# Performance work log

Measured on AMD Instinct MI355X. Metric: run time of the kernel, lower is better.

The kernel has to match this reference:

```python
import jax, jax.numpy as jnp
import numpy as np

N = 100000
E = 1600000
IN_C, HID_C, OUT_C = 512, 256, 64
K = 10
ALPHA = 0.1


def setup_inputs() -> dict:
    key = jax.random.key(0)
    k1, k2, k3, k4 = jax.random.split(key, 4)
    x = jax.random.normal(k1, (N, IN_C), dtype=jnp.float32)
    edge_index = jax.random.randint(k2, (2, E), 0, N, dtype=jnp.int64)
    # Glorot-ish scaled linear weights
    W1 = jax.random.normal(k3, (HID_C, IN_C), dtype=jnp.float32) / np.sqrt(IN_C)
    b1 = jnp.zeros((HID_C,), dtype=jnp.float32)
    W2 = jax.random.normal(k4, (OUT_C, HID_C), dtype=jnp.float32) / np.sqrt(HID_C)
    b2 = jnp.zeros((OUT_C,), dtype=jnp.float32)
    # PPR init: temp[k] = alpha*(1-alpha)^k, temp[K] = (1-alpha)^K
    temp = ALPHA * (1.0 - ALPHA) ** np.arange(K + 1)
    temp[-1] = (1.0 - ALPHA) ** K
    temp = jnp.asarray(temp, dtype=jnp.float32)
    return {"x": x, "edge_index": edge_index, "W1": W1, "b1": b1,
            "W2": W2, "b2": b2, "temp": temp}


def _gcn_norm(edge_index, num_nodes):
    # add self loops with weight 1, symmetric normalization D^-1/2 A D^-1/2
    loop = jnp.arange(num_nodes, dtype=edge_index.dtype)
    src = jnp.concatenate([edge_index[0], loop])
    dst = jnp.concatenate([edge_index[1], loop])
    w = jnp.ones(src.shape[0], dtype=jnp.float32)
    deg = jax.ops.segment_sum(w, dst, num_segments=num_nodes)
    dinv = jnp.where(deg > 0, jax.lax.rsqrt(deg), 0.0)
    norm = dinv[src] * w * dinv[dst]
    return src, dst, norm


def reference(x, edge_index, W1, b1, W2, b2, temp):
    # MLP (inference mode: dropout is identity)
    h = jax.nn.relu(x @ W1.T + b1)
    h = h @ W2.T + b2  # [N, OUT_C]

    src, dst, norm = _gcn_norm(edge_index, N)
    norm = norm[:, None]

    def step(carry, gamma):
        xk, hidden = carry
        xk = jax.ops.segment_sum(norm * xk[src], dst, num_segments=N)
        hidden = hidden + gamma * xk
        return (xk, hidden), None

    hidden0 = temp[0] * h
    (_, hidden), _ = jax.lax.scan(step, (h, hidden0), temp[1:])
    return hidden
```

## Files before the change

### kernel.cpp

```cpp
#include <hip/hip_runtime.h>

#define IN_C   512
#define HID_C  256
#define OUT_C  64
#define KSTEPS 10

typedef __attribute__((ext_vector_type(8))) short bf16x8;
typedef __attribute__((ext_vector_type(4))) float f32x4;

__device__ __forceinline__ uint f2bf(float f) {
    uint u = __float_as_uint(f);
    return (u + 0x7fffu + ((u >> 16) & 1u)) >> 16;
}
__device__ __forceinline__ float bfl(uint u) { return __uint_as_float(u << 16); }
__device__ __forceinline__ float bfh(uint u) { return __uint_as_float(u & 0xffff0000u); }

__global__ void k_init(int* __restrict__ cnt, int* __restrict__ fill, int n) {
    int i = blockIdx.x * blockDim.x + threadIdx.x;
    if (i < n) { cnt[i] = 0; fill[i] = 0; }
}

__global__ void k_hist(const int* __restrict__ ei, int* __restrict__ cnt, int E) {
    int e = blockIdx.x * blockDim.x + threadIdx.x;
    if (e < E) atomicAdd(&cnt[ei[E + e]], 1);
}

__global__ void k_dinv(const int* __restrict__ cnt, float* __restrict__ dinv, int n) {
    int i = blockIdx.x * blockDim.x + threadIdx.x;
    if (i < n) dinv[i] = rsqrtf((float)cnt[i] + 1.0f);
}

__global__ void k_scan1(const int* __restrict__ cnt, int* __restrict__ rowptr,
                        int* __restrict__ bsum, int n) {
    __shared__ int sh[256];
    int i = blockIdx.x * 256 + threadIdx.x;
    int v = (i < n) ? cnt[i] : 0;
    sh[threadIdx.x] = v;
    __syncthreads();
    for (int off = 1; off < 256; off <<= 1) {
        int t = (threadIdx.x >= off) ? sh[threadIdx.x - off] : 0;
        __syncthreads();
        sh[threadIdx.x] += t;
        __syncthreads();
    }
    if (i < n) rowptr[i + 1] = sh[threadIdx.x];
    if (threadIdx.x == 255) bsum[blockIdx.x] = sh[255];
}

__global__ void k_scan2(int* __restrict__ bsum, int nb) {
    __shared__ int sh[512];
    int t = threadIdx.x;
    int v = (t < nb) ? bsum[t] : 0;
    sh[t] = v;
    __syncthreads();
    for (int off = 1; off < 512; off <<= 1) {
        int u = (t >= off) ? sh[t - off] : 0;
        __syncthreads();
        sh[t] += u;
        __syncthreads();
    }
    int ex = (t == 0) ? 0 : sh[t - 1];
    if (t < nb) bsum[t] = ex;
}

__global__ void k_scan3(int* __restrict__ rowptr, const int* __restrict__ bsum, int n) {
    int i = blockIdx.x * blockDim.x + threadIdx.x;
    if (i < n) rowptr[i + 1] += bsum[i >> 8];
    if (i == 0) rowptr[0] = 0;
}

__global__ void k_scatter(const int* __restrict__ ei, const float* __restrict__ dinv,
                          const int* __restrict__ rowptr, int* __restrict__ fill,
                          int2* __restrict__ edges, int E) {
    int e = blockIdx.x * blockDim.x + threadIdx.x;
    if (e < E) {
        int s = ei[e], d = ei[E + e];
        float nv = dinv[s] * dinv[d];
        int pos = rowptr[d] + atomicAdd(&fill[d], 1);
        edges[pos] = make_int2(s, __float_as_int(nv));
    }
}

__global__ void k_cvt(const float* __restrict__ src, ushort* __restrict__ dst, int n) {
    int i = blockIdx.x * blockDim.x + threadIdx.x;
    if (i < n) dst[i] = (ushort)f2bf(src[i]);
}

__global__ __launch_bounds__(256, 4) void k_mlp(
    const float* __restrict__ x, const ushort* __restrict__ W1b,
    const float* __restrict__ b1, const ushort* __restrict__ W2b,
    const float* __restrict__ b2, const float* __restrict__ temp,
    ushort* __restrict__ h, float* __restrict__ out, int n)
{
    __shared__ uint4 smem4[2560];
    char* smem = (char*)smem4;

    const int tid = threadIdx.x;
    const int lane = tid & 63;
    const int w    = tid >> 6;
    const int l15  = lane & 15;
    const int l4   = lane >> 4;
    const int row0 = blockIdx.x * 64;

    f32x4 acc[4][4];
#pragma unroll
    for (int i = 0; i < 4; ++i)
#pragma unroll
        for (int j = 0; j < 4; ++j) acc[i][j] = (f32x4){0.f, 0.f, 0.f, 0.f};

    for (int k0 = 0; k0 < IN_C; k0 += 64) {
#pragma unroll
        for (int it = 0; it < 4; ++it) {
            int f  = tid + it * 256;
            int r  = f >> 4;
            int c4 = f & 15;
            int gr = row0 + r; if (gr >= n) gr = n - 1;
            float4 v = *(const float4*)(x + (size_t)gr * IN_C + k0 + c4 * 4);
            uint p0 = f2bf(v.x) | (f2bf(v.y) << 16);
            uint p1 = f2bf(v.z) | (f2bf(v.w) << 16);
            int boff = (c4 * 8) ^ ((r & 7) << 4);
            *(uint2*)(smem + 32768 + r * 128 + boff) = make_uint2(p0, p1);
        }
#pragma unroll
        for (int it = 0; it < 8; ++it) {
            int m  = tid + it * 256;
            int nn = m >> 3, b = m & 7;
            uint4 v = *(const uint4*)(W1b + (size_t)nn * IN_C + k0 + b * 8);
            int bd = b ^ (nn & 7);
            *(uint4*)(smem + nn * 128 + (bd << 4)) = v;
        }
        __syncthreads();
#pragma unroll
        for (int kk = 0; kk < 2; ++kk) {
            bf16x8 af[4], bfr[4];
            int kb = kk * 4 + l4;
#pragma unroll
            for (int rf = 0; rf < 4; ++rf) {
                int r = rf * 16 + l15;
                af[rf] = *(const bf16x8*)(smem + 32768 + r * 128 + ((kb ^ (r & 7)) << 4));
            }
#pragma unroll
            for (int nf = 0; nf < 4; ++nf) {
                int nn = w * 64 + nf * 16 + l15;
                bfr[nf] = *(const bf16x8*)(smem + nn * 128 + ((kb ^ (nn & 7)) << 4));
            }
#pragma unroll
            for (int rf = 0; rf < 4; ++rf)
#pragma unroll
                for (int nf = 0; nf < 4; ++nf)
                    acc[rf][nf] = __builtin_amdgcn_mfma_f32_16x16x32_bf16(
                        af[rf], bfr[nf], acc[rf][nf], 0, 0, 0);
        }
        __syncthreads();
    }

    float bias1[4];
#pragma unroll
    for (int nf = 0; nf < 4; ++nf) bias1[nf] = b1[w * 64 + nf * 16 + l15];
#pragma unroll
    for (int rf = 0; rf < 4; ++rf)
#pragma unroll
        for (int nf = 0; nf < 4; ++nf)
#pragma unroll
            for (int j = 0; j < 4; ++j) {
                int r = rf * 16 + l4 * 4 + j;
                int c = w * 64 + nf * 16 + l15;
                float v = fmaxf(acc[rf][nf][j] + bias1[nf], 0.f);
                int byte = r * 512 + ((((c >> 3) ^ (r & 7))) << 4) + (c & 7) * 2;
                *(ushort*)(smem + byte) = (ushort)f2bf(v);
            }
    __syncthreads();

    f32x4 acc2[4];
#pragma unroll
    for (int nf = 0; nf < 4; ++nf) acc2[nf] = (f32x4){0.f, 0.f, 0.f, 0.f};
#pragma unroll
    for (int kk = 0; kk < 8; ++kk) {
        int r = w * 16 + l15;
        int kb = kk * 4 + l4;
        bf16x8 a = *(const bf16x8*)(smem + r * 512 + ((kb ^ (r & 7)) << 4));
#pragma unroll
        for (int nf = 0; nf < 4; ++nf) {
            bf16x8 bb = *(const bf16x8*)(W2b + (size_t)(nf * 16 + l15) * HID_C + kb * 8);
            acc2[nf] = __builtin_amdgcn_mfma_f32_16x16x32_bf16(a, bb, acc2[nf], 0, 0, 0);
        }
    }

    float t0 = temp[0];
#pragma unroll
    for (int nf = 0; nf < 4; ++nf) {
        int c = nf * 16 + l15;
        float bias = b2[c];
#pragma unroll
        for (int j = 0; j < 4; ++j) {
            int gr = row0 + w * 16 + l4 * 4 + j;
            if (gr < n) {
                float v = acc2[nf][j] + bias;
                h[(size_t)gr * OUT_C + c]   = (ushort)f2bf(v);
                out[(size_t)gr * OUT_C + c] = t0 * v;
            }
        }
    }
}

__global__ __launch_bounds__(256) void k_prop(
    const int* __restrict__ rowptr, const int2* __restrict__ edges,
    const ushort* __restrict__ cur, ushort* __restrict__ nxt,
    float* __restrict__ out, const float* __restrict__ dinv,
    const float* __restrict__ temp, int k, int n)
{
    const int lane = threadIdx.x & 63;
    const int g    = lane >> 3;
    const int sl   = lane & 7;
    const int wid  = (blockIdx.x * blockDim.x + threadIdx.x) >> 6;
    const int nw   = (gridDim.x * blockDim.x) >> 6;
    const float gamma = temp[k];

    for (int d = wid; d < n; d += nw) {
        const int b = rowptr[d], en = rowptr[d + 1];
        const float di = dinv[d];
        float a[8] = {0.f, 0.f, 0.f, 0.f, 0.f, 0.f, 0.f, 0.f};

        if (g == 0) {
            uint4 raw = *(const uint4*)(cur + (size_t)d * OUT_C + sl * 8);
            float s = di * di;
            a[0] = s * bfl(raw.x); a[1] = s * bfh(raw.x);
            a[2] = s * bfl(raw.y); a[3] = s * bfh(raw.y);
            a[4] = s * bfl(raw.z); a[5] = s * bfh(raw.z);
            a[6] = s * bfl(raw.w); a[7] = s * bfh(raw.w);
        }

        for (int i = b + g; i < en; i += 8) {
            int2 e = edges[i];
            float wv = __int_as_float(e.y);
            uint4 raw = *(const uint4*)(cur + (size_t)e.x * OUT_C + sl * 8);
            a[0] = fmaf(wv, bfl(raw.x), a[0]); a[1] = fmaf(wv, bfh(raw.x), a[1]);
            a[2] = fmaf(wv, bfl(raw.y), a[2]); a[3] = fmaf(wv, bfh(raw.y), a[3]);
            a[4] = fmaf(wv, bfl(raw.z), a[4]); a[5] = fmaf(wv, bfh(raw.z), a[5]);
            a[6] = fmaf(wv, bfl(raw.w), a[6]); a[7] = fmaf(wv, bfh(raw.w), a[7]);
        }

#pragma unroll
        for (int j = 0; j < 8; ++j) {
            a[j] += __shfl_xor(a[j], 8);
            a[j] += __shfl_xor(a[j], 16);
            a[j] += __shfl_xor(a[j], 32);
        }

        if (g == 0) {
            size_t o = (size_t)d * OUT_C + sl * 8;
            uint4 pk;
            pk.x = f2bf(a[0]) | (f2bf(a[1]) << 16);
            pk.y = f2bf(a[2]) | (f2bf(a[3]) << 16);
            pk.z = f2bf(a[4]) | (f2bf(a[5]) << 16);
            pk.w = f2bf(a[6]) | (f2bf(a[7]) << 16);
            *(uint4*)(nxt + o) = pk;
            float4* op = (float4*)(out + o);
            float4 v0 = op[0], v1 = op[1];
            v0.x += gamma * a[0]; v0.y += gamma * a[1];
            v0.z += gamma * a[2]; v0.w += gamma * a[3];
            v1.x += gamma * a[4]; v1.y += gamma * a[5];
            v1.z += gamma * a[6]; v1.w += gamma * a[7];
            op[0] = v0; op[1] = v1;
        }
    }
}

extern "C" void kernel_launch(void* const* d_in, const int* in_sizes, int n_in,
                              void* d_out, int out_size, void* d_ws, size_t ws_size,
                              hipStream_t stream)
{
    const float* x    = (const float*)d_in[0];
    const int*   ei   = (const int*)d_in[1];
    const float* W1   = (const float*)d_in[2];
    const float* b1   = (const float*)d_in[3];
    const float* W2   = (const float*)d_in[4];
    const float* b2   = (const float*)d_in[5];
    const float* temp = (const float*)d_in[6];
    float* out = (float*)d_out;

    const int N = in_sizes[0] / IN_C;
    const int E = in_sizes[1] / 2;

    char* ws = (char*)d_ws;
    ushort* bufA  = (ushort*)ws;
    ushort* bufB  = bufA + (size_t)N * OUT_C;
    int2*   edges = (int2*)(bufB + (size_t)N * OUT_C);
    ushort* W1b   = (ushort*)(edges + E);
    ushort* W2b   = W1b + HID_C * IN_C;
    float*  dinv  = (float*)(W2b + OUT_C * HID_C);
    int*    cnt    = (int*)(dinv + N);
    int*    fill   = cnt + N;
    int*    rowptr = fill + N;
    int*    bsum   = rowptr + (N + 16);

    const int nbN = (N + 255) / 256;
    const int nbE = (E + 255) / 256;

    k_init   <<<nbN, 256, 0, stream>>>(cnt, fill, N);
    k_hist   <<<nbE, 256, 0, stream>>>(ei, cnt, E);
    k_dinv   <<<nbN, 256, 0, stream>>>(cnt, dinv, N);
    k_scan1  <<<nbN, 256, 0, stream>>>(cnt, rowptr, bsum, N);
    k_scan2  <<<1,   512, 0, stream>>>(bsum, nbN);
    k_scan3  <<<nbN, 256, 0, stream>>>(rowptr, bsum, N);
    k_scatter<<<nbE, 256, 0, stream>>>(ei, dinv, rowptr, fill, edges, E);
    k_cvt    <<<(HID_C * IN_C + 255) / 256, 256, 0, stream>>>(W1, W1b, HID_C * IN_C);
    k_cvt    <<<(OUT_C * HID_C + 255) / 256, 256, 0, stream>>>(W2, W2b, OUT_C * HID_C);

    k_mlp<<<(N + 63) / 64, 256, 0, stream>>>(x, W1b, b1, W2b, b2, temp, bufA, out, N);

    ushort* cur = bufA;
    ushort* nxt = bufB;
    for (int k = 1; k <= KSTEPS; ++k) {
        k_prop<<<2048, 256, 0, stream>>>(rowptr, edges, cur, nxt, out, dinv, temp, k, N);
        ushort* t = cur; cur = nxt; nxt = t;
    }
}
```

Measured before the change: 730.9 us.

## Restructure propagation to a node per 8-lane group and halve output updates

The propagation kernel now gives each 8-lane group its own destination node instead of spreading one node across a whole wave. This removes the cross-group shuffle reduction, and the edge loop is unrolled by two to keep more gathers in flight. The fp32 output read-modify-write now runs only on even steps, adding the previous step's features (read from the bf16 buffer) and the current ones together. The last step skips writing the next-feature buffer. The MLP kernel also prefetches the next x/W1 tile into registers and reads W2 from a transposed layout, at the cost of more register pressure and slightly different rounding of the accumulated terms.

```diff
diff --git a/kernel.cpp b/kernel.cpp
--- a/kernel.cpp
+++ b/kernel.cpp
@@ -86,9 +86,19 @@
     if (i < n) dst[i] = (ushort)f2bf(src[i]);
 }
 
+__global__ void k_cvtw2(const float* __restrict__ W2, ushort* __restrict__ w2kt) {
+    int i = blockIdx.x * blockDim.x + threadIdx.x;
+    if (i < OUT_C * HID_C) {
+        int o = i >> 8;
+        int c = i & 255;
+        int kb = c >> 3, j = c & 7;
+        w2kt[((size_t)(kb * 64 + o)) * 8 + j] = (ushort)f2bf(W2[i]);
+    }
+}
+
 __global__ __launch_bounds__(256, 4) void k_mlp(
     const float* __restrict__ x, const ushort* __restrict__ W1b,
-    const float* __restrict__ b1, const ushort* __restrict__ W2b,
+    const float* __restrict__ b1, const ushort* __restrict__ w2kt,
     const float* __restrict__ b2, const float* __restrict__ temp,
     ushort* __restrict__ h, float* __restrict__ out, int n)
 {
@@ -108,28 +118,51 @@
 #pragma unroll
         for (int j = 0; j < 4; ++j) acc[i][j] = (f32x4){0.f, 0.f, 0.f, 0.f};
 
+    float4 px[4];
+    uint4  pw[8];
+#pragma unroll
+    for (int it = 0; it < 4; ++it) {
+        int f = tid + it * 256, r = f >> 4, c4 = f & 15;
+        int gr = row0 + r; if (gr >= n) gr = n - 1;
+        px[it] = *(const float4*)(x + (size_t)gr * IN_C + c4 * 4);
+    }
+#pragma unroll
+    for (int it = 0; it < 8; ++it) {
+        int m = tid + it * 256, nn = m >> 3, bq = m & 7;
+        pw[it] = *(const uint4*)(W1b + (size_t)nn * IN_C + bq * 8);
+    }
+
     for (int k0 = 0; k0 < IN_C; k0 += 64) {
 #pragma unroll
         for (int it = 0; it < 4; ++it) {
-            int f  = tid + it * 256;
-            int r  = f >> 4;
-            int c4 = f & 15;
-            int gr = row0 + r; if (gr >= n) gr = n - 1;
-            float4 v = *(const float4*)(x + (size_t)gr * IN_C + k0 + c4 * 4);
-            uint p0 = f2bf(v.x) | (f2bf(v.y) << 16);
-            uint p1 = f2bf(v.z) | (f2bf(v.w) << 16);
+            int f = tid + it * 256, r = f >> 4, c4 = f & 15;
+            uint p0 = f2bf(px[it].x) | (f2bf(px[it].y) << 16);
+            uint p1 = f2bf(px[it].z) | (f2bf(px[it].w) << 16);
             int boff = (c4 * 8) ^ ((r & 7) << 4);
             *(uint2*)(smem + 32768 + r * 128 + boff) = make_uint2(p0, p1);
         }
 #pragma unroll
         for (int it = 0; it < 8; ++it) {
-            int m  = tid + it * 256;
-            int nn = m >> 3, b = m & 7;
-            uint4 v = *(const uint4*)(W1b + (size_t)nn * IN_C + k0 + b * 8);
-            int bd = b ^ (nn & 7);
-            *(uint4*)(smem + nn * 128 + (bd << 4)) = v;
-        }
-        __syncthreads();
+            int m = tid + it * 256, nn = m >> 3, bq = m & 7;
+            int bd = bq ^ (nn & 7);
+            *(uint4*)(smem + nn * 128 + (bd << 4)) = pw[it];
+        }
+        __syncthreads();
+
+        if (k0 + 64 < IN_C) {
+#pragma unroll
+            for (int it = 0; it < 4; ++it) {
+                int f = tid + it * 256, r = f >> 4, c4 = f & 15;
+                int gr = row0 + r; if (gr >= n) gr = n - 1;
+                px[it] = *(const float4*)(x + (size_t)gr * IN_C + (k0 + 64) + c4 * 4);
+            }
+#pragma unroll
+            for (int it = 0; it < 8; ++it) {
+                int m = tid + it * 256, nn = m >> 3, bq = m & 7;
+                pw[it] = *(const uint4*)(W1b + (size_t)nn * IN_C + (k0 + 64) + bq * 8);
+            }
+        }
+
 #pragma unroll
         for (int kk = 0; kk < 2; ++kk) {
             bf16x8 af[4], bfr[4];
@@ -181,7 +214,7 @@
         bf16x8 a = *(const bf16x8*)(smem + r * 512 + ((kb ^ (r & 7)) << 4));
 #pragma unroll
         for (int nf = 0; nf < 4; ++nf) {
-            bf16x8 bb = *(const bf16x8*)(W2b + (size_t)(nf * 16 + l15) * HID_C + kb * 8);
+            bf16x8 bb = *(const bf16x8*)(w2kt + ((size_t)kb * 64 + nf * 16 + l15) * 8);
             acc2[nf] = __builtin_amdgcn_mfma_f32_16x16x32_bf16(a, bb, acc2[nf], 0, 0, 0);
         }
     }
@@ -207,61 +240,75 @@
     const int* __restrict__ rowptr, const int2* __restrict__ edges,
     const ushort* __restrict__ cur, ushort* __restrict__ nxt,
     float* __restrict__ out, const float* __restrict__ dinv,
-    const float* __restrict__ temp, int k, int n)
+    const float* __restrict__ temp, int kcur, int do_rmw, int do_nxt, int n)
 {
     const int lane = threadIdx.x & 63;
     const int g    = lane >> 3;
     const int sl   = lane & 7;
     const int wid  = (blockIdx.x * blockDim.x + threadIdx.x) >> 6;
     const int nw   = (gridDim.x * blockDim.x) >> 6;
-    const float gamma = temp[k];
-
-    for (int d = wid; d < n; d += nw) {
-        const int b = rowptr[d], en = rowptr[d + 1];
-        const float di = dinv[d];
-        float a[8] = {0.f, 0.f, 0.f, 0.f, 0.f, 0.f, 0.f, 0.f};
-
-        if (g == 0) {
-            uint4 raw = *(const uint4*)(cur + (size_t)d * OUT_C + sl * 8);
-            float s = di * di;
-            a[0] = s * bfl(raw.x); a[1] = s * bfh(raw.x);
-            a[2] = s * bfl(raw.y); a[3] = s * bfh(raw.y);
-            a[4] = s * bfl(raw.z); a[5] = s * bfh(raw.z);
-            a[6] = s * bfl(raw.w); a[7] = s * bfh(raw.w);
-        }
-
-        for (int i = b + g; i < en; i += 8) {
+    const float gc = temp[kcur];
+    const float gp = temp[kcur - 1];
+
+    for (int base = wid * 8; base < n; base += nw * 8) {
+        int d = base + g;
+        bool act = d < n;
+        int dd = act ? d : (n - 1);
+        int b = rowptr[dd];
+        int en = act ? rowptr[dd + 1] : b;
+        float di = dinv[dd];
+        size_t rowoff = (size_t)dd * OUT_C + sl * 8;
+
+        uint4 sraw = *(const uint4*)(cur + rowoff);
+        float c0 = bfl(sraw.x), c1 = bfh(sraw.x), c2 = bfl(sraw.y), c3 = bfh(sraw.y),
+              c4 = bfl(sraw.z), c5 = bfh(sraw.z), c6 = bfl(sraw.w), c7 = bfh(sraw.w);
+        float s = di * di;
+        float a0 = s * c0, a1 = s * c1, a2 = s * c2, a3 = s * c3,
+              a4 = s * c4, a5 = s * c5, a6 = s * c6, a7 = s * c7;
+
+        int i = b;
+        for (; i + 2 <= en; i += 2) {
+            int2 e0 = edges[i], e1 = edges[i + 1];
+            uint4 r0 = *(const uint4*)(cur + (size_t)e0.x * OUT_C + sl * 8);
+            uint4 r1 = *(const uint4*)(cur + (size_t)e1.x * OUT_C + sl * 8);
+            float w0 = __int_as_float(e0.y), w1 = __int_as_float(e1.y);
+            a0 = fmaf(w0, bfl(r0.x), a0); a1 = fmaf(w0, bfh(r0.x), a1);
+            a2 = fmaf(w0, bfl(r0.y), a2); a3 = fmaf(w0, bfh(r0.y), a3);
+            a4 = fmaf(w0, bfl(r0.z), a4); a5 = fmaf(w0, bfh(r0.z), a5);
+            a6 = fmaf(w0, bfl(r0.w), a6); a7 = fmaf(w0, bfh(r0.w), a7);
+            a0 = fmaf(w1, bfl(r1.x), a0); a1 = fmaf(w1, bfh(r1.x), a1);
+            a2 = fmaf(w1, bfl(r1.y), a2); a3 = fmaf(w1, bfh(r1.y), a3);
+            a4 = fmaf(w1, bfl(r1.z), a4); a5 = fmaf(w1, bfh(r1.z), a5);
+            a6 = fmaf(w1, bfl(r1.w), a6); a7 = fmaf(w1, bfh(r1.w), a7);
+        }
+        if (i < en) {
             int2 e = edges[i];
-            float wv = __int_as_float(e.y);
-            uint4 raw = *(const uint4*)(cur + (size_t)e.x * OUT_C + sl * 8);
-            a[0] = fmaf(wv, bfl(raw.x), a[0]); a[1] = fmaf(wv, bfh(raw.x), a[1]);
-            a[2] = fmaf(wv, bfl(raw.y), a[2]); a[3] = fmaf(wv, bfh(raw.y), a[3]);
-            a[4] = fmaf(wv, bfl(raw.z), a[4]); a[5] = fmaf(wv, bfh(raw.z), a[5]);
-            a[6] = fmaf(wv, bfl(raw.w), a[6]); a[7] = fmaf(wv, bfh(raw.w), a[7]);
-        }
-
-#pragma unroll
-        for (int j = 0; j < 8; ++j) {
-            a[j] += __shfl_xor(a[j], 8);
-            a[j] += __shfl_xor(a[j], 16);
-            a[j] += __shfl_xor(a[j], 32);
-        }
-
-        if (g == 0) {
-            size_t o = (size_t)d * OUT_C + sl * 8;
-            uint4 pk;
-            pk.x = f2bf(a[0]) | (f2bf(a[1]) << 16);
-            pk.y = f2bf(a[2]) | (f2bf(a[3]) << 16);
-            pk.z = f2bf(a[4]) | (f2bf(a[5]) << 16);
-            pk.w = f2bf(a[6]) | (f2bf(a[7]) << 16);
-            *(uint4*)(nxt + o) = pk;
-            float4* op = (float4*)(out + o);
-            float4 v0 = op[0], v1 = op[1];
-            v0.x += gamma * a[0]; v0.y += gamma * a[1];
-            v0.z += gamma * a[2]; v0.w += gamma * a[3];
-            v1.x += gamma * a[4]; v1.y += gamma * a[5];
-            v1.z += gamma * a[6]; v1.w += gamma * a[7];
-            op[0] = v0; op[1] = v1;
+            uint4 r0 = *(const uint4*)(cur + (size_t)e.x * OUT_C + sl * 8);
+            float w0 = __int_as_float(e.y);
+            a0 = fmaf(w0, bfl(r0.x), a0); a1 = fmaf(w0, bfh(r0.x), a1);
+            a2 = fmaf(w0, bfl(r0.y), a2); a3 = fmaf(w0, bfh(r0.y), a3);
+            a4 = fmaf(w0, bfl(r0.z), a4); a5 = fmaf(w0, bfh(r0.z), a5);
+            a6 = fmaf(w0, bfl(r0.w), a6); a7 = fmaf(w0, bfh(r0.w), a7);
+        }
+
+        if (act) {
+            if (do_nxt) {
+                uint4 pk;
+                pk.x = f2bf(a0) | (f2bf(a1) << 16);
+                pk.y = f2bf(a2) | (f2bf(a3) << 16);
+                pk.z = f2bf(a4) | (f2bf(a5) << 16);
+                pk.w = f2bf(a6) | (f2bf(a7) << 16);
+                *(uint4*)(nxt + rowoff) = pk;
+            }
+            if (do_rmw) {
+                float4* op = (float4*)(out + rowoff);
+                float4 v0 = op[0], v1 = op[1];
+                v0.x += gp * c0 + gc * a0; v0.y += gp * c1 + gc * a1;
+                v0.z += gp * c2 + gc * a2; v0.w += gp * c3 + gc * a3;
+                v1.x += gp * c4 + gc * a4; v1.y += gp * c5 + gc * a5;
+                v1.z += gp * c6 + gc * a6; v1.w += gp * c7 + gc * a7;
+                op[0] = v0; op[1] = v1;
+            }
         }
     }
 }
@@ -287,8 +334,8 @@
     ushort* bufB  = bufA + (size_t)N * OUT_C;
     int2*   edges = (int2*)(bufB + (size_t)N * OUT_C);
     ushort* W1b   = (ushort*)(edges + E);
-    ushort* W2b   = W1b + HID_C * IN_C;
-    float*  dinv  = (float*)(W2b + OUT_C * HID_C);
+    ushort* w2kt  = W1b + HID_C * IN_C;
+    float*  dinv  = (float*)(w2kt + OUT_C * HID_C);
     int*    cnt    = (int*)(dinv + N);
     int*    fill   = cnt + N;
     int*    rowptr = fill + N;
@@ -305,14 +352,17 @@
     k_scan3  <<<nbN, 256, 0, stream>>>(rowptr, bsum, N);
     k_scatter<<<nbE, 256, 0, stream>>>(ei, dinv, rowptr, fill, edges, E);
     k_cvt    <<<(HID_C * IN_C + 255) / 256, 256, 0, stream>>>(W1, W1b, HID_C * IN_C);
-    k_cvt    <<<(OUT_C * HID_C + 255) / 256, 256, 0, stream>>>(W2, W2b, OUT_C * HID_C);
-
-    k_mlp<<<(N + 63) / 64, 256, 0, stream>>>(x, W1b, b1, W2b, b2, temp, bufA, out, N);
+    k_cvtw2  <<<(OUT_C * HID_C + 255) / 256, 256, 0, stream>>>(W2, w2kt);
+
+    k_mlp<<<(N + 63) / 64, 256, 0, stream>>>(x, W1b, b1, w2kt, b2, temp, bufA, out, N);
 
     ushort* cur = bufA;
     ushort* nxt = bufB;
     for (int k = 1; k <= KSTEPS; ++k) {
-        k_prop<<<2048, 256, 0, stream>>>(rowptr, edges, cur, nxt, out, dinv, temp, k, N);
+        int do_rmw = (k % 2 == 0) ? 1 : 0;
+        int do_nxt = (k < KSTEPS) ? 1 : 0;
+        k_prop<<<2048, 256, 0, stream>>>(rowptr, edges, cur, nxt, out, dinv,
+                                         temp, k, do_rmw, do_nxt, N);
         ushort* t = cur; cur = nxt; nxt = t;
     }
 }
```

Measured after the change: 832.7 us. 1.14x slower.
